# Optimization experiments

Hardware: AMD Instinct MI355X
Metric: run time of the kernel (lower is better)

Reference implementation:

```python
import jax, jax.numpy as jnp
import numpy as np

N_ITER = 10
N_PRIMAL = 5
N_IONS = 1
B, H, W, A = 1, 96, 96, 60
D = H  # detector bins == H, forced by the reshape in the original code


def _conv(x, w, b):
    y = jax.lax.conv_general_dilated(x, w, (1, 1), [(1, 1), (1, 1)],
                                     dimension_numbers=('NCHW', 'OIHW', 'NCHW'))
    return y + b[None, :, None, None]


def _prelu(x, a):
    return jnp.where(x >= 0, x, a * x)


def _block(x, w1, b1, a1, w2, b2, a2, w3, b3):
    x = _prelu(_conv(x, w1, b1), a1)
    x = _prelu(_conv(x, w2, b2), a2)
    return _conv(x, w3, b3)


def setup_inputs():
    key = jax.random.key(0)
    ks = jax.random.split(key, 12)
    s = 0.05
    dc = 3 * N_IONS      # DualNet input channels
    pc = N_PRIMAL + 1    # PrimalNet input channels
    inp = {
        'dual': jax.random.normal(ks[0], (B, N_IONS, A, D), jnp.float32),
        'primal': jax.random.normal(ks[1], (B, N_PRIMAL, H, W, 1), jnp.float32),
        'g': jax.random.normal(ks[2], (B, N_IONS, A, D), jnp.float32),
        'sysm_angles': jax.random.normal(ks[3], (B, A, H * W, N_IONS * D), jnp.float32) * s,
        'sysm_angles_norm': jax.random.normal(ks[4], (B, A, N_IONS * H, H * W), jnp.float32) * s,
        'dual_w1': jax.random.normal(ks[5], (N_ITER, 32, dc, 3, 3), jnp.float32) * s,
        'dual_b1': jnp.zeros((N_ITER, 32), jnp.float32),
        'dual_a1': jnp.full((N_ITER,), 0.25, jnp.float32),
        'dual_w2': jax.random.normal(ks[6], (N_ITER, 32, 32, 3, 3), jnp.float32) * s,
        'dual_b2': jnp.zeros((N_ITER, 32), jnp.float32),
        'dual_a2': jnp.full((N_ITER,), 0.25, jnp.float32),
        'dual_w3': jax.random.normal(ks[7], (N_ITER, N_IONS, 32, 3, 3), jnp.float32) * s,
        'dual_b3': jnp.zeros((N_ITER, N_IONS), jnp.float32),
        'primal_w1': jax.random.normal(ks[8], (N_ITER, 32, pc, 3, 3), jnp.float32) * s,
        'primal_b1': jnp.zeros((N_ITER, 32), jnp.float32),
        'primal_a1': jnp.full((N_ITER,), 0.25, jnp.float32),
        'primal_w2': jax.random.normal(ks[9], (N_ITER, 32, 32, 3, 3), jnp.float32) * s,
        'primal_b2': jnp.zeros((N_ITER, 32), jnp.float32),
        'primal_a2': jnp.full((N_ITER,), 0.25, jnp.float32),
        'primal_w3': jax.random.normal(ks[10], (N_ITER, N_PRIMAL, 32, 3, 3), jnp.float32) * s,
        'primal_b3': jnp.zeros((N_ITER, N_PRIMAL), jnp.float32),
        'return_all': 0,
    }
    return inp


def _forward(dual, primal, g, sysm_angles, sysm_angles_norm,
             dw1, db1, da1, dw2, db2, da2, dw3, db3,
             pw1, pb1, pa1, pw2, pb2, pa2, pw3, pb3):
    for k in range(N_ITER):
        # forward projection: fortran-flatten primal channel 1 (index h + H*w), batched over all angles
        img_f = primal[:, 1, :, :, 0].transpose(0, 2, 1).reshape(B, H * W)   # [B, H*W]
        prod = jnp.einsum('bamn,bn->bam', sysm_angles_norm, img_f)           # [B, A, N_IONS*H]
        evalop1 = prod.reshape(B, A, H, N_IONS).transpose(0, 3, 1, 2)        # [B, N_IONS, A, D]
        x = jnp.concatenate([dual, evalop1, g], axis=1)
        dual = dual + _block(x, dw1[k], db1[k], da1[k], dw2[k], db2[k], da2[k], dw3[k], db3[k])
        # adjoint (back-projection) summed over angles
        dual2 = dual.transpose(0, 2, 3, 1).reshape(B, A, D * N_IONS)         # [B, A, D*N_IONS]
        vec = jnp.einsum('bavn,ban->bv', sysm_angles, dual2)                 # [B, H*W]
        evalop2 = vec.reshape(B, W, H).transpose(0, 2, 1)[:, None]           # [B, 1, H, W] fortran unflatten
        p2d = primal[..., 0]                                                 # [B, N_PRIMAL, H, W]
        xp = jnp.concatenate([p2d, evalop2], axis=1)
        p2d = p2d + _block(xp, pw1[k], pb1[k], pa1[k], pw2[k], pb2[k], pa2[k], pw3[k], pb3[k])
        primal = p2d[..., None]
    return primal[:, 0:1]  # [B, 1, H, W, 1]


def reference(dual, primal, g, sysm_angles, sysm_angles_norm,
              dual_w1, dual_b1, dual_a1, dual_w2, dual_b2, dual_a2, dual_w3, dual_b3,
              primal_w1, primal_b1, primal_a1, primal_w2, primal_b2, primal_a2, primal_w3, primal_b3,
              return_all):
    return _forward(dual, primal, g, sysm_angles, sysm_angles_norm,
                    dual_w1, dual_b1, dual_a1, dual_w2, dual_b2, dual_a2, dual_w3, dual_b3,
                    primal_w1, primal_b1, primal_a1, primal_w2, primal_b2, primal_a2, primal_w3, primal_b3)
```

## Files before the change

### kernel.cpp

```cpp
#include <hip/hip_runtime.h>

#define AA 60
#define HH 96
#define WW 96
#define DD 96
#define HWP (HH * WW)
#define ADP (AA * DD)
#define NITER 10
#define MATEL (60 * 96 * 9216)

typedef unsigned short ushort8 __attribute__((ext_vector_type(8)));

__device__ inline float b2f(unsigned short u) {
    return __uint_as_float(((unsigned)u) << 16);
}
__device__ inline unsigned short f2b(float f) {
    unsigned u = __float_as_uint(f);
    u += 0x7FFFu + ((u >> 16) & 1u);
    return (unsigned short)(u >> 16);
}

__global__ __launch_bounds__(256) void cvt_kernel(const float* __restrict__ a,
                                                  const float* __restrict__ b,
                                                  ushort8* __restrict__ da,
                                                  ushort8* __restrict__ db, int n8) {
    int stride = gridDim.x * 256;
    for (int i = blockIdx.x * 256 + threadIdx.x; i < 2 * n8; i += stride) {
        const float* src; ushort8* dst; int j;
        if (i < n8) { src = a; dst = da; j = i; }
        else        { src = b; dst = db; j = i - n8; }
        float4 x = reinterpret_cast<const float4*>(src)[2 * j];
        float4 y = reinterpret_cast<const float4*>(src)[2 * j + 1];
        ushort8 o;
        o[0] = f2b(x.x); o[1] = f2b(x.y); o[2] = f2b(x.z); o[3] = f2b(x.w);
        o[4] = f2b(y.x); o[5] = f2b(y.y); o[6] = f2b(y.z); o[7] = f2b(y.w);
        dst[j] = o;
    }
}

__global__ __launch_bounds__(256) void init_kernel(const float* __restrict__ dual,
                            const float* __restrict__ g,
                            const float* __restrict__ primal,
                            float* __restrict__ xd, float* __restrict__ xp,
                            float* __restrict__ imgf, float* __restrict__ xp5) {
    int i = blockIdx.x * 256 + threadIdx.x;
    if (i < ADP) { xd[i] = dual[i]; xd[2 * ADP + i] = g[i]; }
    if (i < 5 * HWP) xp[i] = primal[i];
    if (i < HWP) {
        imgf[(i % WW) * HH + i / WW] = primal[HWP + i];
        xp5[i] = 0.f;
    }
}

__global__ __launch_bounds__(256) void einsum1_kernel(const unsigned short* __restrict__ norm,
                               const float* __restrict__ imgf,
                               float* __restrict__ out) {
    int row  = blockIdx.x * 4 + (threadIdx.x >> 6);
    int lane = threadIdx.x & 63;
    const unsigned short* mr = norm + (size_t)row * HWP;
    float s = 0.f;
    for (int k = 0; k < HWP / 512; ++k) {
        int n = 8 * lane + 512 * k;
        ushort8 m8 = *reinterpret_cast<const ushort8*>(mr + n);
        float4 i0 = *reinterpret_cast<const float4*>(imgf + n);
        float4 i1 = *reinterpret_cast<const float4*>(imgf + n + 4);
        s += b2f(m8[0]) * i0.x + b2f(m8[1]) * i0.y + b2f(m8[2]) * i0.z + b2f(m8[3]) * i0.w
           + b2f(m8[4]) * i1.x + b2f(m8[5]) * i1.y + b2f(m8[6]) * i1.z + b2f(m8[7]) * i1.w;
    }
#pragma unroll
    for (int off = 32; off > 0; off >>= 1) s += __shfl_down(s, off);
    if (lane == 0) out[row] = s;
}

__global__ __launch_bounds__(256) void einsum2_kernel(const unsigned short* __restrict__ sysm,
                               const float* __restrict__ xd,
                               float* __restrict__ xp5) {
    __shared__ float sd[4 * DD];
    int t  = threadIdx.x;
    int a0 = (blockIdx.x % 15) * 4;
    int v  = (blockIdx.x / 15) * 256 + t;
    for (int j = t; j < 4 * DD; j += 256) sd[j] = xd[a0 * DD + j];
    __syncthreads();
    float s = 0.f;
    for (int ai = 0; ai < 4; ++ai) {
        const unsigned short* row = sysm + ((size_t)(a0 + ai) * HWP + v) * DD;
        const float* dl = sd + ai * DD;
#pragma unroll
        for (int jj = 0; jj < DD / 8; ++jj) {
            ushort8 m8 = *reinterpret_cast<const ushort8*>(row + 8 * jj);
            s += b2f(m8[0]) * dl[8 * jj]     + b2f(m8[1]) * dl[8 * jj + 1]
               + b2f(m8[2]) * dl[8 * jj + 2] + b2f(m8[3]) * dl[8 * jj + 3]
               + b2f(m8[4]) * dl[8 * jj + 4] + b2f(m8[5]) * dl[8 * jj + 5]
               + b2f(m8[6]) * dl[8 * jj + 6] + b2f(m8[7]) * dl[8 * jj + 7];
        }
    }
    atomicAdd(xp5 + (v % HH) * WW + (v / HH), s);
}

template <int CIN, int NOUT>
__global__ __launch_bounds__(64) void conv_mid(
        const float* __restrict__ in,
        const float* __restrict__ wgt,
        const float* __restrict__ bias,
        const float* __restrict__ alpha,
        float* __restrict__ out,
        int Hc, int Wc) {
    int hw  = Hc * Wc;
    int pix = blockIdx.x * 64 + threadIdx.x;
    int y = pix / Wc, x = pix % Wc;
    int oc0 = blockIdx.y * NOUT;
    const float* wb = wgt + (size_t)oc0 * CIN * 9;
    float a = alpha[0];
    float acc[NOUT];
#pragma unroll
    for (int o = 0; o < NOUT; ++o) acc[o] = bias[oc0 + o];
    for (int ci = 0; ci < CIN; ++ci) {
        const float* ip = in + ci * hw;
#pragma unroll
        for (int ky = 0; ky < 3; ++ky) {
            int yy = y + ky - 1;
            bool yok = (unsigned)yy < (unsigned)Hc;
#pragma unroll
            for (int kx = 0; kx < 3; ++kx) {
                int xx = x + kx - 1;
                bool vok = yok && ((unsigned)xx < (unsigned)Wc);
                float v = ip[vok ? yy * Wc + xx : 0];
                v = vok ? v : 0.f;
#pragma unroll
                for (int o = 0; o < NOUT; ++o)
                    acc[o] += wb[(o * CIN + ci) * 9 + ky * 3 + kx] * v;
            }
        }
    }
#pragma unroll
    for (int o = 0; o < NOUT; ++o) {
        float r = acc[o];
        r = (r >= 0.f) ? r : a * r;
        out[(oc0 + o) * hw + pix] = r;
    }
}

__global__ __launch_bounds__(64) void conv3d_last(const float* __restrict__ in,
        const float* __restrict__ wgt,
        const float* __restrict__ bias,
        float* __restrict__ xd) {
    int pix = blockIdx.x * 64 + threadIdx.x;
    int y = pix / DD, x = pix % DD;
    int c0 = blockIdx.y * 8;
    float r = (blockIdx.y == 0) ? bias[0] : 0.f;
    for (int ci = c0; ci < c0 + 8; ++ci) {
        const float* ip = in + ci * ADP;
#pragma unroll
        for (int ky = 0; ky < 3; ++ky) {
            int yy = y + ky - 1;
            bool yok = (unsigned)yy < (unsigned)AA;
#pragma unroll
            for (int kx = 0; kx < 3; ++kx) {
                int xx = x + kx - 1;
                bool vok = yok && ((unsigned)xx < (unsigned)DD);
                float v = ip[vok ? yy * DD + xx : 0];
                v = vok ? v : 0.f;
                r += wgt[ci * 9 + ky * 3 + kx] * v;
            }
        }
    }
    atomicAdd(xd + pix, r);
}

__global__ __launch_bounds__(64) void conv3p_last(const float* __restrict__ in,
        const float* __restrict__ wgt,
        const float* __restrict__ bias,
        float* __restrict__ xp, float* __restrict__ imgf,
        float* __restrict__ xp5, float* __restrict__ dout, int fin) {
    int pix = blockIdx.x * 64 + threadIdx.x;
    int y = pix / WW, x = pix % WW;
    int oc = blockIdx.y;
    const float* wb = wgt + (size_t)oc * 32 * 9;
    float r = bias[oc];
    for (int ci = 0; ci < 32; ++ci) {
        const float* ip = in + ci * HWP;
#pragma unroll
        for (int ky = 0; ky < 3; ++ky) {
            int yy = y + ky - 1;
            bool yok = (unsigned)yy < (unsigned)HH;
#pragma unroll
            for (int kx = 0; kx < 3; ++kx) {
                int xx = x + kx - 1;
                bool vok = yok && ((unsigned)xx < (unsigned)WW);
                float v = ip[vok ? yy * WW + xx : 0];
                v = vok ? v : 0.f;
                r += wb[ci * 9 + ky * 3 + kx] * v;
            }
        }
    }
    float nv = xp[oc * HWP + pix] + r;
    xp[oc * HWP + pix] = nv;
    if (oc == 1) imgf[x * HH + y] = nv;
    if (oc == 2) xp5[pix] = 0.f;
    if (fin && oc == 0) dout[pix] = nv;
}

extern "C" void kernel_launch(void* const* d_in, const int* in_sizes, int n_in,
                              void* d_out, int out_size, void* d_ws, size_t ws_size,
                              hipStream_t stream) {
    const float* dual   = (const float*)d_in[0];
    const float* primal = (const float*)d_in[1];
    const float* g      = (const float*)d_in[2];
    const float* sysm   = (const float*)d_in[3];
    const float* norm   = (const float*)d_in[4];
    const float* dw1 = (const float*)d_in[5];
    const float* db1 = (const float*)d_in[6];
    const float* da1 = (const float*)d_in[7];
    const float* dw2 = (const float*)d_in[8];
    const float* db2 = (const float*)d_in[9];
    const float* da2 = (const float*)d_in[10];
    const float* dw3 = (const float*)d_in[11];
    const float* db3 = (const float*)d_in[12];
    const float* pw1 = (const float*)d_in[13];
    const float* pb1 = (const float*)d_in[14];
    const float* pa1 = (const float*)d_in[15];
    const float* pw2 = (const float*)d_in[16];
    const float* pb2 = (const float*)d_in[17];
    const float* pa2 = (const float*)d_in[18];
    const float* pw3 = (const float*)d_in[19];
    const float* pb3 = (const float*)d_in[20];

    unsigned short* normb = (unsigned short*)d_ws;
    unsigned short* sysmb = normb + MATEL;
    float* xd   = (float*)(sysmb + MATEL);
    float* xp   = xd + 3 * ADP;
    float* imgf = xp + 6 * HWP;
    float* h1   = imgf + HWP;
    float* h2   = h1 + 32 * ADP;
    float* g1   = h2 + 32 * ADP;
    float* g2   = g1 + 32 * HWP;

    cvt_kernel<<<4096, 256, 0, stream>>>(norm, sysm, (ushort8*)normb, (ushort8*)sysmb, MATEL / 8);
    init_kernel<<<(5 * HWP + 255) / 256, 256, 0, stream>>>(dual, g, primal, xd, xp, imgf, xp + 5 * HWP);

    for (int k = 0; k < NITER; ++k) {
        einsum1_kernel<<<ADP / 4, 256, 0, stream>>>(normb, imgf, xd + ADP);
        conv_mid<3, 4><<<dim3(ADP / 64, 8), 64, 0, stream>>>(
            xd, dw1 + k * 32 * 3 * 9, db1 + k * 32, da1 + k, h1, AA, DD);
        conv_mid<32, 4><<<dim3(ADP / 64, 8), 64, 0, stream>>>(
            h1, dw2 + k * 32 * 32 * 9, db2 + k * 32, da2 + k, h2, AA, DD);
        conv3d_last<<<dim3(ADP / 64, 4), 64, 0, stream>>>(
            h2, dw3 + k * 32 * 9, db3 + k, xd);
        einsum2_kernel<<<15 * 36, 256, 0, stream>>>(sysmb, xd, xp + 5 * HWP);
        conv_mid<6, 4><<<dim3(HWP / 64, 8), 64, 0, stream>>>(
            xp, pw1 + k * 32 * 6 * 9, pb1 + k * 32, pa1 + k, g1, HH, WW);
        conv_mid<32, 4><<<dim3(HWP / 64, 8), 64, 0, stream>>>(
            g1, pw2 + k * 32 * 32 * 9, pb2 + k * 32, pa2 + k, g2, HH, WW);
        conv3p_last<<<dim3(HWP / 64, 5), 64, 0, stream>>>(
            g2, pw3 + k * 5 * 32 * 9, pb3 + k * 5, xp, imgf, xp + 5 * HWP,
            (float*)d_out, k == NITER - 1 ? 1 : 0);
    }
}
```

Before: 1.224 ms.

## Transpose sysm during bf16 conversion for coalesced einsum2 reads

The sysm conversion now writes a transposed bf16 layout [A][D][pixel], with the Fortran pixel permutation folded in, staged through LDS. einsum2 then reads contiguous pixels per detector bin, so each wave's loads are coalesced instead of each thread striding over its own 192-byte row, and each thread accumulates four output pixels. The conversion kernels are split into chunked launches and use nontemporal loads. The transpose adds LDS traffic and 2-byte strided LDS accesses to the one-time conversion.

```diff
diff --git a/kernel.cpp b/kernel.cpp
--- a/kernel.cpp
+++ b/kernel.cpp
@@ -10,6 +10,8 @@
 #define MATEL (60 * 96 * 9216)
 
 typedef unsigned short ushort8 __attribute__((ext_vector_type(8)));
+typedef unsigned short ushort4v __attribute__((ext_vector_type(4)));
+typedef float float4v __attribute__((ext_vector_type(4)));
 
 __device__ inline float b2f(unsigned short u) {
     return __uint_as_float(((unsigned)u) << 16);
@@ -20,21 +22,48 @@
     return (unsigned short)(u >> 16);
 }
 
-__global__ __launch_bounds__(256) void cvt_kernel(const float* __restrict__ a,
-                                                  const float* __restrict__ b,
-                                                  ushort8* __restrict__ da,
-                                                  ushort8* __restrict__ db, int n8) {
-    int stride = gridDim.x * 256;
-    for (int i = blockIdx.x * 256 + threadIdx.x; i < 2 * n8; i += stride) {
-        const float* src; ushort8* dst; int j;
-        if (i < n8) { src = a; dst = da; j = i; }
-        else        { src = b; dst = db; j = i - n8; }
-        float4 x = reinterpret_cast<const float4*>(src)[2 * j];
-        float4 y = reinterpret_cast<const float4*>(src)[2 * j + 1];
-        ushort8 o;
-        o[0] = f2b(x.x); o[1] = f2b(x.y); o[2] = f2b(x.z); o[3] = f2b(x.w);
-        o[4] = f2b(y.x); o[5] = f2b(y.y); o[6] = f2b(y.z); o[7] = f2b(y.w);
-        dst[j] = o;
+__global__ __launch_bounds__(256) void cvtA_kernel(const float* __restrict__ src,
+                                                   ushort8* __restrict__ dst,
+                                                   int base, int n8) {
+    int i = base + blockIdx.x * 256 + threadIdx.x;
+    if (i >= n8) return;
+    const float4v* s = reinterpret_cast<const float4v*>(src) + 2 * (size_t)i;
+    float4v x = __builtin_nontemporal_load(s);
+    float4v y = __builtin_nontemporal_load(s + 1);
+    ushort8 o;
+    o[0] = f2b(x[0]); o[1] = f2b(x[1]); o[2] = f2b(x[2]); o[3] = f2b(x[3]);
+    o[4] = f2b(y[0]); o[5] = f2b(y[1]); o[6] = f2b(y[2]); o[7] = f2b(y[3]);
+    dst[i] = o;
+}
+
+__global__ __launch_bounds__(256) void cvtB_kernel(const float* __restrict__ sysm,
+                                                   unsigned short* __restrict__ sysmT,
+                                                   int a_base) {
+    __shared__ unsigned short lds[96][132];
+    int a  = a_base + blockIdx.y;
+    int p0 = blockIdx.x * 128;
+    int t  = threadIdx.x;
+    int p_local = t >> 1, half = t & 1;
+    int p = p0 + p_local;
+    int v = (p % 96) * 96 + p / 96;
+    const float* srow = sysm + ((size_t)a * HWP + v) * DD + half * 48;
+#pragma unroll
+    for (int jj = 0; jj < 12; ++jj) {
+        float4v x = __builtin_nontemporal_load(reinterpret_cast<const float4v*>(srow) + jj);
+        int n = half * 48 + 4 * jj;
+        lds[n][p_local]     = f2b(x[0]);
+        lds[n + 1][p_local] = f2b(x[1]);
+        lds[n + 2][p_local] = f2b(x[2]);
+        lds[n + 3][p_local] = f2b(x[3]);
+    }
+    __syncthreads();
+    int l = t & 63, wv = t >> 6;
+    unsigned short* obase = sysmT + (size_t)a * DD * HWP + p0;
+#pragma unroll
+    for (int pass = 0; pass < 24; ++pass) {
+        int n = pass * 4 + wv;
+        unsigned val = (unsigned)lds[n][2 * l] | ((unsigned)lds[n][2 * l + 1] << 16);
+        *reinterpret_cast<unsigned*>(obase + (size_t)n * HWP + 2 * l) = val;
     }
 }
 
@@ -72,29 +101,33 @@
     if (lane == 0) out[row] = s;
 }
 
-__global__ __launch_bounds__(256) void einsum2_kernel(const unsigned short* __restrict__ sysm,
+__global__ __launch_bounds__(64) void einsum2_kernel(const unsigned short* __restrict__ sysmT,
                                const float* __restrict__ xd,
                                float* __restrict__ xp5) {
     __shared__ float sd[4 * DD];
     int t  = threadIdx.x;
-    int a0 = (blockIdx.x % 15) * 4;
-    int v  = (blockIdx.x / 15) * 256 + t;
-    for (int j = t; j < 4 * DD; j += 256) sd[j] = xd[a0 * DD + j];
+    int a0 = blockIdx.y * 4;
+    int p0 = blockIdx.x * 256 + t * 4;
+    for (int j = t; j < 4 * DD; j += 64) sd[j] = xd[a0 * DD + j];
     __syncthreads();
-    float s = 0.f;
+    float a0c = 0.f, a1c = 0.f, a2c = 0.f, a3c = 0.f;
     for (int ai = 0; ai < 4; ++ai) {
-        const unsigned short* row = sysm + ((size_t)(a0 + ai) * HWP + v) * DD;
+        const unsigned short* base = sysmT + ((size_t)(a0 + ai) * DD) * HWP + p0;
         const float* dl = sd + ai * DD;
-#pragma unroll
-        for (int jj = 0; jj < DD / 8; ++jj) {
-            ushort8 m8 = *reinterpret_cast<const ushort8*>(row + 8 * jj);
-            s += b2f(m8[0]) * dl[8 * jj]     + b2f(m8[1]) * dl[8 * jj + 1]
-               + b2f(m8[2]) * dl[8 * jj + 2] + b2f(m8[3]) * dl[8 * jj + 3]
-               + b2f(m8[4]) * dl[8 * jj + 4] + b2f(m8[5]) * dl[8 * jj + 5]
-               + b2f(m8[6]) * dl[8 * jj + 6] + b2f(m8[7]) * dl[8 * jj + 7];
-        }
-    }
-    atomicAdd(xp5 + (v % HH) * WW + (v / HH), s);
+#pragma unroll 8
+        for (int n = 0; n < DD; ++n) {
+            ushort4v m4 = *reinterpret_cast<const ushort4v*>(base + (size_t)n * HWP);
+            float d = dl[n];
+            a0c += b2f(m4[0]) * d;
+            a1c += b2f(m4[1]) * d;
+            a2c += b2f(m4[2]) * d;
+            a3c += b2f(m4[3]) * d;
+        }
+    }
+    atomicAdd(xp5 + p0,     a0c);
+    atomicAdd(xp5 + p0 + 1, a1c);
+    atomicAdd(xp5 + p0 + 2, a2c);
+    atomicAdd(xp5 + p0 + 3, a3c);
 }
 
 template <int CIN, int NOUT>
@@ -226,8 +259,8 @@
     const float* pb3 = (const float*)d_in[20];
 
     unsigned short* normb = (unsigned short*)d_ws;
-    unsigned short* sysmb = normb + MATEL;
-    float* xd   = (float*)(sysmb + MATEL);
+    unsigned short* sysmT = normb + MATEL;
+    float* xd   = (float*)(sysmT + MATEL);
     float* xp   = xd + 3 * ADP;
     float* imgf = xp + 6 * HWP;
     float* h1   = imgf + HWP;
@@ -235,7 +268,12 @@
     float* g1   = h2 + 32 * ADP;
     float* g2   = g1 + 32 * HWP;
 
-    cvt_kernel<<<4096, 256, 0, stream>>>(norm, sysm, (ushort8*)normb, (ushort8*)sysmb, MATEL / 8);
+    const int N8 = MATEL / 8;
+    const int CH = N8 / 4;
+    for (int c = 0; c < 4; ++c)
+        cvtA_kernel<<<CH / 256, 256, 0, stream>>>(norm, (ushort8*)normb, c * CH, N8);
+    for (int c = 0; c < 5; ++c)
+        cvtB_kernel<<<dim3(HWP / 128, 12), 256, 0, stream>>>(sysm, sysmT, c * 12);
     init_kernel<<<(5 * HWP + 255) / 256, 256, 0, stream>>>(dual, g, primal, xd, xp, imgf, xp + 5 * HWP);
 
     for (int k = 0; k < NITER; ++k) {
@@ -246,7 +284,7 @@
             h1, dw2 + k * 32 * 32 * 9, db2 + k * 32, da2 + k, h2, AA, DD);
         conv3d_last<<<dim3(ADP / 64, 4), 64, 0, stream>>>(
             h2, dw3 + k * 32 * 9, db3 + k, xd);
-        einsum2_kernel<<<15 * 36, 256, 0, stream>>>(sysmb, xd, xp + 5 * HWP);
+        einsum2_kernel<<<dim3(HWP / 256, 15), 64, 0, stream>>>(sysmT, xd, xp + 5 * HWP);
         conv_mid<6, 4><<<dim3(HWP / 64, 8), 64, 0, stream>>>(
             xp, pw1 + k * 32 * 6 * 9, pb1 + k * 32, pa1 + k, g1, HH, WW);
         conv_mid<32, 4><<<dim3(HWP / 64, 8), 64, 0, stream>>>(
```

Result: slower. 1.265 ms (+3.3%).
